# Performance work log

Measured on AMD Instinct MI355X. Metric: run time of the kernel, lower is better.

The kernel has to match this reference:

```python
import jax, jax.numpy as jnp
import numpy as np

D, H, C = 128, 128, 10
N, M, T = 256, 128, 128
DELTA = 1.0
SIGMA2 = 1.0
JITTER = 1e-3


def _net(params, x):
    # x: (D,) -> (C,)   2-hidden-layer tanh MLP (the `network` of NTKSVGP)
    W1, b1, W2, b2, W3, b3 = params
    h = jnp.tanh(x @ W1 + b1)
    h = jnp.tanh(h @ W2 + b2)
    return h @ W3 + b3


def _flat_jac(params, X):
    # per-sample jacobian wrt all params, flattened over params: (B, C, P)
    jac = jax.vmap(lambda x: jax.jacrev(_net)(params, x))(X)
    leaves = jax.tree_util.tree_leaves(jac)
    return jnp.concatenate([j.reshape(j.shape[0], j.shape[1], -1) for j in leaves], axis=-1)


def _forward(X, Y, Z, X_test, W1, b1, W2, b2, W3, b3):
    params = (W1, b1, W2, b2, W3, b3)
    scale = 1.0 / (DELTA * N)  # build_ntk: 1/(delta*num_data)

    Jx = _flat_jac(params, X)       # (N, C, P)
    Jz = _flat_jac(params, Z)       # (M, C, P)
    Jt = _flat_jac(params, X_test)  # (T, C, P)

    Kzx = jnp.einsum('mcp,ncp->cmn', Jz, Jx) * scale   # (C, M, N)
    Kzz = jnp.einsum('mcp,kcp->cmk', Jz, Jz) * scale   # (C, M, M)

    # Gaussian likelihood duals: beta = 2*Hessian = I/sigma2, alpha = -d nll/df = (Y-F)/sigma2
    F = jax.vmap(_net, in_axes=(None, 0))(params, X)   # (N, C)
    beta_diag = jnp.ones_like(F) / SIGMA2              # (N, C)
    alpha = (Y - F) / SIGMA2
    Lam = alpha + F * beta_diag                        # calc_lambda

    # beta_u = Kzx diag(beta) Kzx^T ; Lambda_u = Kzx Lambda
    beta_u = jnp.einsum('cmn,nc,ckn->cmk', Kzx, beta_diag, Kzx)  # (C, M, M)
    Lambda_u = jnp.einsum('cmn,nc->cm', Kzx, Lam)                # (C, M)

    Iz = jnp.eye(M, dtype=Kzz.dtype)
    Kzz_j = Kzz + JITTER * Iz
    KzzB = Kzz_j + beta_u + JITTER * Iz
    alpha_u = jnp.linalg.solve(KzzB, Lambda_u[..., None])[..., 0]  # (C, M)

    # predict_from_sparse_duals (full_cov=False branch)
    Lm = jnp.linalg.cholesky(Kzz_j)  # lower, batched over C
    Lb = jnp.linalg.cholesky(KzzB)
    Kxz = jnp.einsum('tcp,mcp->ctm', Jt, Jz) * scale  # (C, T, M)
    Kxx_diag = jnp.einsum('tcp,tcp->ct', Jt, Jt) * scale  # (C, T)

    f_mean = jnp.einsum('ctm,cm->tc', Kxz, alpha_u)   # (T, C)
    Kzxt = jnp.swapaxes(Kxz, -1, -2)                  # (C, M, T)
    Am = jax.scipy.linalg.solve_triangular(Lm, Kzxt, lower=True)
    Ab = jax.scipy.linalg.solve_triangular(Lb, Kzxt, lower=True)
    f_var = Kxx_diag - jnp.sum(Am * Am, axis=-2) + jnp.sum(Ab * Ab, axis=-2)  # (C, T)
    return jnp.stack([f_mean, f_var.T])  # (2, T, C)


def setup_inputs() -> dict:
    key = jax.random.key(0)
    ks = jax.random.split(key, 8)
    return {
        'X': jax.random.normal(ks[0], (N, D), jnp.float32),
        'Y': jax.random.normal(ks[1], (N, C), jnp.float32),
        'Z': jax.random.normal(ks[2], (M, D), jnp.float32),
        'X_test': jax.random.normal(ks[3], (T, D), jnp.float32),
        'W1': jax.random.normal(ks[4], (D, H), jnp.float32) / np.sqrt(D),
        'b1': jnp.zeros((H,), jnp.float32),
        'W2': jax.random.normal(ks[5], (H, H), jnp.float32) / np.sqrt(H),
        'b2': jnp.zeros((H,), jnp.float32),
        'W3': jax.random.normal(ks[6], (H, C), jnp.float32) / np.sqrt(H),
        'b3': jnp.zeros((C,), jnp.float32),
    }


def reference(X, Y, Z, X_test, W1, b1, W2, b2, W3, b3):
    return _forward(X, Y, Z, X_test, W1, b1, W2, b2, W3, b3)
```

## Files before the change

### kernel.cpp

```cpp
#include <hip/hip_runtime.h>

#define H 128
#define DD 128
#define CC 10
#define NX 256
#define MZ 128
#define TN 128
#define S_TOT 512
#define SCALE (1.0f/256.0f)
#define JIT 1e-3f
#define INV_S2 1.0f

#define OFF_XS    0u
#define OFF_A1    (OFF_XS   + S_TOT*DD)
#define OFF_A2    (OFF_A1   + S_TOT*H)
#define OFF_G1    (OFF_A2   + S_TOT*H)
#define OFF_G2    (OFF_G1   + S_TOT*CC*H)
#define OFF_BASE  (OFF_G2   + S_TOT*CC*H)
#define BASE_ZX   0u
#define BASE_ZZ   (3u*MZ*NX)
#define BASE_TZ   (3u*MZ*NX + 3u*MZ*MZ)
#define OFF_KZX   (OFF_BASE + 3u*MZ*NX + 3u*MZ*MZ + 3u*TN*MZ)
#define OFF_KZZ   (OFF_KZX  + CC*MZ*NX)
#define OFF_KXZ   (OFF_KZZ  + CC*MZ*MZ)
#define OFF_KZZJ  (OFF_KXZ  + CC*TN*MZ)
#define OFF_KZZB  (OFF_KZZJ + CC*MZ*MZ)
#define OFF_LAMU  (OFF_KZZB + CC*MZ*MZ)
#define OFF_LC    (OFF_LAMU + CC*MZ)
#define OFF_INVD  (OFF_LC   + 2u*CC*MZ*MZ)
#define OFF_YLAM  (OFF_INVD + 2u*CC*MZ)

#define WRED(val, qi) { float v_ = (val);                                     \
  v_ += __shfl_down(v_,32,64); v_ += __shfl_down(v_,16,64);                   \
  v_ += __shfl_down(v_, 8,64); v_ += __shfl_down(v_, 4,64);                   \
  v_ += __shfl_down(v_, 2,64); v_ += __shfl_down(v_, 1,64);                   \
  if ((h & 63) == 0) partG[(qi)*2 + (h>>6)] = v_; }

__global__ __launch_bounds__(128) void k_features(
    const float* __restrict__ X, const float* __restrict__ Z, const float* __restrict__ Xt,
    const float* __restrict__ W1, const float* __restrict__ b1,
    const float* __restrict__ W2, const float* __restrict__ b2,
    const float* __restrict__ W3,
    float* __restrict__ XS, float* __restrict__ A1, float* __restrict__ A2,
    float* __restrict__ G1, float* __restrict__ G2, float* __restrict__ LamU,
    float* __restrict__ out)
{
  int s = blockIdx.x, h = threadIdx.x;
  __shared__ float xs[DD], a1s[H], g2s[CC*H];
  __shared__ float w2t[H*129];
  __shared__ float partG[46];
  if (s == 0) {
    #pragma unroll
    for (int c = 0; c < CC; ++c) LamU[c*MZ + h] = 0.0f;
  }
  const float* xin = (s < NX) ? X + s*DD : (s < NX+MZ ? Z + (s-NX)*DD : Xt + (s-NX-MZ)*DD);
  float xv = xin[h];
  xs[h] = xv; XS[s*DD + h] = xv;
  {
    const float4* W2_4 = (const float4*)W2;
    #pragma unroll 4
    for (int it = 0; it < 32; ++it) {
      int f = it*128 + h;
      int r = f >> 5;
      int q = f & 31;
      float4 v = W2_4[f];
      w2t[(4*q+0)*129 + r] = v.x;
      w2t[(4*q+1)*129 + r] = v.y;
      w2t[(4*q+2)*129 + r] = v.z;
      w2t[(4*q+3)*129 + r] = v.w;
    }
  }
  __syncthreads();
  float acc = b1[h];
  #pragma unroll 8
  for (int d0 = 0; d0 < DD; ++d0) acc += xs[d0] * W1[d0*H + h];
  float a1 = tanhf(acc);
  a1s[h] = a1; A1[s*H + h] = a1;
  __syncthreads();
  acc = b2[h];
  #pragma unroll 8
  for (int d0 = 0; d0 < H; ++d0) acc += a1s[d0] * w2t[h*129 + d0];
  float a2 = tanhf(acc);
  A2[s*H + h] = a2;
  float t2 = 1.0f - a2*a2;
  float g2v[CC];
  #pragma unroll
  for (int c = 0; c < CC; ++c) {
    g2v[c] = W3[h*CC + c] * t2;
    g2s[c*H + h] = g2v[c];
    G2[(s*CC + c)*H + h] = g2v[c];
  }
  __syncthreads();
  float t1 = 1.0f - a1*a1;
  float accs[CC];
  #pragma unroll
  for (int c = 0; c < CC; ++c) accs[c] = 0.0f;
  #pragma unroll 4
  for (int k = 0; k < H; ++k) {
    float w = w2t[k*129 + h];
    #pragma unroll
    for (int c = 0; c < CC; ++c) accs[c] += w * g2s[c*H + k];
  }
  #pragma unroll
  for (int c = 0; c < CC; ++c) G1[(s*CC + c)*H + h] = t1 * accs[c];
  if (s >= NX + MZ) {
    int t = s - NX - MZ;
    WRED(xv*xv, 0) WRED(a1*a1, 1) WRED(a2*a2, 2)
    #pragma unroll
    for (int c = 0; c < CC; ++c) {
      float g1v = t1 * accs[c];
      WRED(g1v*g1v, 3+2*c)
      WRED(g2v[c]*g2v[c], 4+2*c)
    }
    __syncthreads();
    if (h < CC) {
      int c = h;
      float nx  = partG[0] + partG[1];
      float na1 = partG[2] + partG[3];
      float na2 = partG[4] + partG[5];
      float n1 = partG[(3+2*c)*2] + partG[(3+2*c)*2+1];
      float n2 = partG[(4+2*c)*2] + partG[(4+2*c)*2+1];
      out[TN*CC + t*CC + c] = SCALE * ((1.0f+nx)*n1 + (1.0f+na1)*n2 + (1.0f+na2));
    }
  }
}

__global__ __launch_bounds__(256) void k_base(const float* __restrict__ XS,
    const float* __restrict__ A1, const float* __restrict__ A2, float* __restrict__ Base)
{
  int set = blockIdx.z;
  int colsN = (set == 0) ? NX : MZ;
  if ((int)blockIdx.x * 16 >= colsN) return;
  int rowOff = (set == 2) ? NX+MZ : NX;
  int colOff = (set == 0) ? 0 : NX;
  unsigned baseOff = (set == 0) ? BASE_ZX : (set == 1 ? BASE_ZZ : BASE_TZ);
  __shared__ float rx[16*132], r1[16*132], r2[16*132], cxs[16*132], c1s[16*132], c2s[16*132];
  int tid = threadIdx.x, m0 = blockIdx.y*16, n0 = blockIdx.x*16;
  for (int idx = tid; idx < 16*128; idx += 256) {
    int r = idx >> 7, hh = idx & 127;
    int sr = rowOff + m0 + r, sc = colOff + n0 + r;
    rx [r*132+hh] = XS[sr*DD+hh]; r1[r*132+hh] = A1[sr*H+hh]; r2[r*132+hh] = A2[sr*H+hh];
    cxs[r*132+hh] = XS[sc*DD+hh]; c1s[r*132+hh] = A1[sc*H+hh]; c2s[r*132+hh] = A2[sc*H+hh];
  }
  __syncthreads();
  int ty = tid >> 4, tx = tid & 15;
  const float4* pa = (const float4*)(rx  + ty*132);
  const float4* pb = (const float4*)(cxs + tx*132);
  const float4* pc = (const float4*)(r1  + ty*132);
  const float4* pd = (const float4*)(c1s + tx*132);
  const float4* pe = (const float4*)(r2  + ty*132);
  const float4* pf = (const float4*)(c2s + tx*132);
  float d0 = 0, d1 = 0, d2 = 0;
  #pragma unroll 8
  for (int q = 0; q < 32; ++q) {
    float4 a = pa[q], b = pb[q]; d0 += a.x*b.x + a.y*b.y + a.z*b.z + a.w*b.w;
    float4 c = pc[q], d = pd[q]; d1 += c.x*d.x + c.y*d.y + c.z*d.z + c.w*d.w;
    float4 e = pe[q], f = pf[q]; d2 += e.x*f.x + e.y*f.y + e.z*f.z + e.w*f.w;
  }
  int m = m0 + ty, n = n0 + tx;
  float* Bp = Base + baseOff;
  int area = 128 * colsN;
  Bp[0*area + m*colsN + n] = 1.0f + d0;
  Bp[1*area + m*colsN + n] = 1.0f + d1;
  Bp[2*area + m*colsN + n] = 1.0f + d2;
}

__global__ __launch_bounds__(256) void k_gram(const float* __restrict__ G1, const float* __restrict__ G2,
    const float* __restrict__ Base, const float* __restrict__ Y,
    float* __restrict__ Kzx, float* __restrict__ Kzz, float* __restrict__ Kxz,
    float* __restrict__ LamU)
{
  int z = blockIdx.z, set = z / CC, c = z % CC;
  int colsN = (set == 0) ? NX : MZ;
  if ((int)blockIdx.x * 16 >= colsN) return;
  int rowOff = (set == 2) ? NX+MZ : NX;
  int colOff = (set == 0) ? 0 : NX;
  unsigned baseOff = (set == 0) ? BASE_ZX : (set == 1 ? BASE_ZZ : BASE_TZ);
  float* outp = (set == 0) ? Kzx + c*MZ*NX : (set == 1 ? Kzz + c*MZ*MZ : Kxz + c*TN*MZ);
  __shared__ float g1r[16*132], g2r[16*132], g1c[16*132], g2c[16*132];
  int tid = threadIdx.x, m0 = blockIdx.y*16, n0 = blockIdx.x*16;
  for (int idx = tid; idx < 2048; idx += 256) {
    int r = idx >> 7, hh = idx & 127;
    int sr = rowOff + m0 + r, sc = colOff + n0 + r;
    g1r[r*132+hh] = G1[(sr*CC + c)*H + hh]; g2r[r*132+hh] = G2[(sr*CC + c)*H + hh];
    g1c[r*132+hh] = G1[(sc*CC + c)*H + hh]; g2c[r*132+hh] = G2[(sc*CC + c)*H + hh];
  }
  __syncthreads();
  int ty = tid >> 4, tx = tid & 15;
  const float4* p1 = (const float4*)(g1r + ty*132);
  const float4* p2 = (const float4*)(g1c + tx*132);
  const float4* p3 = (const float4*)(g2r + ty*132);
  const float4* p4 = (const float4*)(g2c + tx*132);
  float dg1 = 0, dg2 = 0;
  #pragma unroll 8
  for (int q = 0; q < 32; ++q) {
    float4 a = p1[q], b = p2[q]; dg1 += a.x*b.x + a.y*b.y + a.z*b.z + a.w*b.w;
    float4 e = p3[q], f = p4[q]; dg2 += e.x*f.x + e.y*f.y + e.z*f.z + e.w*f.w;
  }
  int m = m0 + ty, n = n0 + tx;
  const float* Bp = Base + baseOff;
  int area = 128 * colsN;
  float b0 = Bp[m*colsN + n], b1v = Bp[area + m*colsN + n], b2v = Bp[2*area + m*colsN + n];
  float val = SCALE * (b0*dg1 + b1v*dg2 + b2v);
  outp[m*colsN + n] = val;
  if (set == 0) {
    float lam = val * Y[n*CC + c] * INV_S2;
    lam += __shfl_xor(lam, 1, 64); lam += __shfl_xor(lam, 2, 64);
    lam += __shfl_xor(lam, 4, 64); lam += __shfl_xor(lam, 8, 64);
    if (tx == 0) atomicAdd(&LamU[c*MZ + m], lam);
  }
}

__global__ __launch_bounds__(256) void k_kzzb(const float* __restrict__ Kzx, const float* __restrict__ Kzz,
    float* __restrict__ Kzzj, float* __restrict__ KzzB)
{
  int c = blockIdx.z, m0 = blockIdx.y*16, k0 = blockIdx.x*16;
  int tid = threadIdx.x, ty = tid >> 4, tx = tid & 15;
  __shared__ float Am[16*260], Ak[16*260];
  const float* Kc = Kzx + c*MZ*NX;
  const float4* src_m = (const float4*)(Kc + m0*NX);
  const float4* src_k = (const float4*)(Kc + k0*NX);
  float4* Am4 = (float4*)Am;
  float4* Ak4 = (float4*)Ak;
  for (int idx = tid; idx < 16*64; idx += 256) {
    int r = idx >> 6, q = idx & 63;
    Am4[r*65 + q] = src_m[r*64 + q];
    Ak4[r*65 + q] = src_k[r*64 + q];
  }
  __syncthreads();
  const float4* am = (const float4*)(Am + ty*260);
  const float4* ak = (const float4*)(Ak + tx*260);
  float acc = 0;
  #pragma unroll 8
  for (int q = 0; q < 64; ++q) {
    float4 a = am[q], b = ak[q];
    acc += a.x*b.x + a.y*b.y + a.z*b.z + a.w*b.w;
  }
  int m = m0+ty, k = k0+tx, idx = c*MZ*MZ + m*MZ + k;
  float kzz = Kzz[idx];
  float dia = (m == k) ? 1.0f : 0.0f;
  Kzzj[idx] = kzz + dia*JIT;
  KzzB[idx] = kzz + acc*INV_S2 + dia*2.0f*JIT;
}

__global__ __launch_bounds__(512) void k_chol(const float* __restrict__ Kzzj, const float* __restrict__ KzzB,
    float* __restrict__ Lc, float* __restrict__ invd,
    const float* __restrict__ LamU, float* __restrict__ ylam)
{
  int which = blockIdx.x & 1, c = blockIdx.x >> 1;
  const float* Ain = (which ? KzzB : Kzzj) + c*MZ*MZ;
  float* LcB = Lc + (size_t)(which*CC + c)*MZ*MZ;
  float* invB = invd + (which*CC + c)*MZ;
  __shared__ float As[MZ*MZ];
  __shared__ float4 pan[MZ];
  __shared__ float bs[MZ];
  __shared__ float ys[MZ];
  int tid = threadIdx.x;
  int rg = tid & 31, kp = tid >> 5;
  float4* As4 = (float4*)As;
  {
    float4* d4 = (float4*)As; const float4* s4 = (const float4*)Ain;
    #pragma unroll
    for (int r = 0; r < 8; ++r) d4[tid + 512*r] = s4[tid + 512*r];
  }
  if (tid < MZ) bs[tid] = which ? LamU[c*MZ + tid] : 0.0f;
  __syncthreads();
  for (int jb = 0; jb < 32; ++jb) {
    int j = jb*4;
    if (tid < MZ) {
      int i = tid;
      float r0 = As[(j+0)*MZ + i], r1 = As[(j+1)*MZ + i], r2 = As[(j+2)*MZ + i], r3 = As[(j+3)*MZ + i];
      float a00 = As[j*MZ+j];
      float a10 = As[j*MZ+j+1], a20 = As[j*MZ+j+2], a30 = As[j*MZ+j+3];
      float a11 = As[(j+1)*MZ+j+1], a21 = As[(j+1)*MZ+j+2], a31 = As[(j+1)*MZ+j+3];
      float a22 = As[(j+2)*MZ+j+2], a32 = As[(j+2)*MZ+j+3];
      float a33 = As[(j+3)*MZ+j+3];
      float bj0 = bs[j], bj1 = bs[j+1], bj2 = bs[j+2], bj3 = bs[j+3];
      float id0 = rsqrtf(a00);
      float l10 = a10*id0, l20 = a20*id0, l30 = a30*id0;
      float id1 = rsqrtf(a11 - l10*l10);
      float l21 = (a21 - l20*l10)*id1, l31 = (a31 - l30*l10)*id1;
      float id2 = rsqrtf(a22 - l20*l20 - l21*l21);
      float l32 = (a32 - l30*l20 - l31*l21)*id2;
      float id3 = rsqrtf(a33 - l30*l30 - l31*l31 - l32*l32);
      float c0 = r0*id0;
      float c1 = (r1 - c0*l10)*id1;
      float c2 = (r2 - c0*l20 - c1*l21)*id2;
      float c3 = (r3 - c0*l30 - c1*l31 - c2*l32)*id3;
      float y0 = bj0*id0;
      float y1 = (bj1 - l10*y0)*id1;
      float y2 = (bj2 - l20*y0 - l21*y1)*id2;
      float y3 = (bj3 - l30*y0 - l31*y1 - l32*y2)*id3;
      pan[i] = make_float4(c0, c1, c2, c3);
      LcB[(j+0)*MZ + i] = (i > j+0) ? c0 : 0.0f;
      LcB[(j+1)*MZ + i] = (i > j+1) ? c1 : 0.0f;
      LcB[(j+2)*MZ + i] = (i > j+2) ? c2 : 0.0f;
      LcB[(j+3)*MZ + i] = (i > j+3) ? c3 : 0.0f;
      if (i == j) {
        invB[j] = id0; invB[j+1] = id1; invB[j+2] = id2; invB[j+3] = id3;
        ys[j] = y0; ys[j+1] = y1; ys[j+2] = y2; ys[j+3] = y3;
      }
      if (i >= j+4) bs[i] -= c0*y0 + c1*y1 + c2*y2 + c3*y3;
    }
    __syncthreads();
    float4 p0 = pan[4*rg+0], p1 = pan[4*rg+1], p2 = pan[4*rg+2], p3 = pan[4*rg+3];
    int kstart = (j + 4) + ((kp - (j + 4)) & 15);
    int kend = 4*rg + 3;
    for (int k = kstart; k <= kend; k += 16) {
      float4 ck = pan[k];
      float4 a4 = As4[k*32 + rg];
      a4.x -= p0.x*ck.x + p0.y*ck.y + p0.z*ck.z + p0.w*ck.w;
      a4.y -= p1.x*ck.x + p1.y*ck.y + p1.z*ck.z + p1.w*ck.w;
      a4.z -= p2.x*ck.x + p2.y*ck.y + p2.z*ck.z + p2.w*ck.w;
      a4.w -= p3.x*ck.x + p3.y*ck.y + p3.z*ck.z + p3.w*ck.w;
      As4[k*32 + rg] = a4;
    }
    __syncthreads();
  }
  if (which && tid < MZ) ylam[c*MZ + tid] = ys[tid];
}

__device__ __forceinline__ float rdlane(float v, int lane) {
  return __int_as_float(__builtin_amdgcn_readlane(__float_as_int(v), lane));
}

__global__ __launch_bounds__(512) void k_solve(const float* __restrict__ Lc,
    const float* __restrict__ invd, const float* __restrict__ ylam,
    const float* __restrict__ Kxz, float* __restrict__ out)
{
  int quarter = blockIdx.x & 3;
  int which   = (blockIdx.x >> 2) & 1;
  int c       = blockIdx.x >> 3;
  const float2* LcB2 = (const float2*)(Lc + (size_t)(which*CC + c)*MZ*MZ);
  const float2* invB2 = (const float2*)(invd + (which*CC + c)*MZ);
  const float2* ylB2  = (const float2*)(ylam + c*MZ);
  int tid = threadIdx.x, l = tid & 63, wv = tid >> 6;
  __shared__ float2 Ls[MZ*64];
  #pragma unroll
  for (int r = 0; r < 16; ++r) Ls[tid + 512*r] = LcB2[tid + 512*r];
  float2 iv = invB2[l];
  float2 yl = ylB2[l];
  int col0 = quarter*32 + wv*4;
  const float* K0 = Kxz + (size_t)c*TN*MZ;
  float2 b0 = *(const float2*)(K0 + (size_t)(col0+0)*MZ + 2*l);
  float2 b1 = *(const float2*)(K0 + (size_t)(col0+1)*MZ + 2*l);
  float2 b2 = *(const float2*)(K0 + (size_t)(col0+2)*MZ + 2*l);
  float2 b3 = *(const float2*)(K0 + (size_t)(col0+3)*MZ + 2*l);
  __syncthreads();
  #pragma unroll
  for (int j = 0; j < MZ; ++j) {
    const int owner = j >> 1;
    float2 Lj = Ls[j*64 + l];
    float y0, y1, y2, y3;
    if ((j & 1) == 0) {
      y0 = rdlane(b0.x * iv.x, owner);
      y1 = rdlane(b1.x * iv.x, owner);
      y2 = rdlane(b2.x * iv.x, owner);
      y3 = rdlane(b3.x * iv.x, owner);
    } else {
      y0 = rdlane(b0.y * iv.y, owner);
      y1 = rdlane(b1.y * iv.y, owner);
      y2 = rdlane(b2.y * iv.y, owner);
      y3 = rdlane(b3.y * iv.y, owner);
    }
    b0.x -= Lj.x * y0; b0.y -= Lj.y * y0;
    b1.x -= Lj.x * y1; b1.y -= Lj.y * y1;
    b2.x -= Lj.x * y2; b2.y -= Lj.y * y2;
    b3.x -= Lj.x * y3; b3.y -= Lj.y * y3;
    if (l == owner) {
      if ((j & 1) == 0) { b0.x = y0; b1.x = y1; b2.x = y2; b3.x = y3; }
      else              { b0.y = y0; b1.y = y1; b2.y = y2; b3.y = y3; }
    }
  }
  float sq0 = b0.x*b0.x + b0.y*b0.y, fm0 = b0.x*yl.x + b0.y*yl.y;
  float sq1 = b1.x*b1.x + b1.y*b1.y, fm1 = b1.x*yl.x + b1.y*yl.y;
  float sq2 = b2.x*b2.x + b2.y*b2.y, fm2 = b2.x*yl.x + b2.y*yl.y;
  float sq3 = b3.x*b3.x + b3.y*b3.y, fm3 = b3.x*yl.x + b3.y*yl.y;
  #pragma unroll
  for (int off = 32; off > 0; off >>= 1) {
    sq0 += __shfl_xor(sq0, off, 64); fm0 += __shfl_xor(fm0, off, 64);
    sq1 += __shfl_xor(sq1, off, 64); fm1 += __shfl_xor(fm1, off, 64);
    sq2 += __shfl_xor(sq2, off, 64); fm2 += __shfl_xor(fm2, off, 64);
    sq3 += __shfl_xor(sq3, off, 64); fm3 += __shfl_xor(fm3, off, 64);
  }
  if (l == 0) {
    float sgn = which ? 1.0f : -1.0f;
    float* var = out + TN*CC;
    atomicAdd(&var[(col0+0)*CC + c], sgn*sq0);
    atomicAdd(&var[(col0+1)*CC + c], sgn*sq1);
    atomicAdd(&var[(col0+2)*CC + c], sgn*sq2);
    atomicAdd(&var[(col0+3)*CC + c], sgn*sq3);
    if (which) {
      out[(col0+0)*CC + c] = fm0;
      out[(col0+1)*CC + c] = fm1;
      out[(col0+2)*CC + c] = fm2;
      out[(col0+3)*CC + c] = fm3;
    }
  }
}

extern "C" void kernel_launch(void* const* d_in, const int* in_sizes, int n_in,
                              void* d_out, int out_size, void* d_ws, size_t ws_size,
                              hipStream_t stream) {
  (void)in_sizes; (void)n_in; (void)out_size; (void)ws_size;
  const float* X  = (const float*)d_in[0];
  const float* Y  = (const float*)d_in[1];
  const float* Z  = (const float*)d_in[2];
  const float* Xt = (const float*)d_in[3];
  const float* W1 = (const float*)d_in[4];
  const float* b1 = (const float*)d_in[5];
  const float* W2 = (const float*)d_in[6];
  const float* b2 = (const float*)d_in[7];
  const float* W3 = (const float*)d_in[8];
  float* ws  = (float*)d_ws;
  float* out = (float*)d_out;

  float* XS   = ws + OFF_XS;
  float* A1   = ws + OFF_A1;
  float* A2   = ws + OFF_A2;
  float* G1   = ws + OFF_G1;
  float* G2   = ws + OFF_G2;
  float* Base = ws + OFF_BASE;
  float* Kzx  = ws + OFF_KZX;
  float* Kzz  = ws + OFF_KZZ;
  float* Kxz  = ws + OFF_KXZ;
  float* Kzzj = ws + OFF_KZZJ;
  float* KzzB = ws + OFF_KZZB;
  float* LamU = ws + OFF_LAMU;
  float* Lc   = ws + OFF_LC;
  float* invd = ws + OFF_INVD;
  float* ylam = ws + OFF_YLAM;

  k_features<<<S_TOT, 128, 0, stream>>>(X, Z, Xt, W1, b1, W2, b2, W3, XS, A1, A2, G1, G2, LamU, out);
  k_base<<<dim3(16, 8, 3), 256, 0, stream>>>(XS, A1, A2, Base);
  k_gram<<<dim3(16, 8, 3*CC), 256, 0, stream>>>(G1, G2, Base, Y, Kzx, Kzz, Kxz, LamU);
  k_kzzb<<<dim3(8, 8, CC), 256, 0, stream>>>(Kzx, Kzz, Kzzj, KzzB);
  k_chol<<<2*CC, 512, 0, stream>>>(Kzzj, KzzB, Lc, invd, LamU, ylam);
  k_solve<<<8*CC, 512, 0, stream>>>(Lc, invd, ylam, Kxz, out);
}
```

Baseline: 120.9 us.

## Process two samples per block in features kernel and 2x2 register tile gram kernel

k_features now handles two samples per 256-thread block, so each block loads and transposes W2 into shared memory once for two samples instead of once per sample. k_gram switches from 16x16 to 32x32 output tiles, with each thread computing a 2x2 block of outputs, so every shared-memory float4 load is reused twice and the number of blocks re-staging G1/G2 rows drops. The cost is more registers and shared memory per block and fewer blocks overall, which may reduce occupancy and parallelism on a GPU with many CUs.

```diff
diff --git a/kernel.cpp b/kernel.cpp
--- a/kernel.cpp
+++ b/kernel.cpp
@@ -36,7 +36,7 @@
   v_ += __shfl_down(v_, 2,64); v_ += __shfl_down(v_, 1,64);                   \
   if ((h & 63) == 0) partG[(qi)*2 + (h>>6)] = v_; }
 
-__global__ __launch_bounds__(128) void k_features(
+__global__ __launch_bounds__(256) void k_features(
     const float* __restrict__ X, const float* __restrict__ Z, const float* __restrict__ Xt,
     const float* __restrict__ W1, const float* __restrict__ b1,
     const float* __restrict__ W2, const float* __restrict__ b2,
@@ -45,22 +45,25 @@
     float* __restrict__ G1, float* __restrict__ G2, float* __restrict__ LamU,
     float* __restrict__ out)
 {
-  int s = blockIdx.x, h = threadIdx.x;
-  __shared__ float xs[DD], a1s[H], g2s[CC*H];
+  int b = blockIdx.x, tid = threadIdx.x;
+  int g = tid >> 7, h = tid & 127;
+  int s = 2*b + g;
   __shared__ float w2t[H*129];
-  __shared__ float partG[46];
-  if (s == 0) {
+  __shared__ float xs[2][DD], a1s[2][H], g2s[2][CC*H];
+  __shared__ float partGA[2][46];
+  float* partG = partGA[g];
+  if (b == 0 && tid < 128) {
     #pragma unroll
-    for (int c = 0; c < CC; ++c) LamU[c*MZ + h] = 0.0f;
+    for (int c = 0; c < CC; ++c) LamU[c*MZ + tid] = 0.0f;
   }
   const float* xin = (s < NX) ? X + s*DD : (s < NX+MZ ? Z + (s-NX)*DD : Xt + (s-NX-MZ)*DD);
   float xv = xin[h];
-  xs[h] = xv; XS[s*DD + h] = xv;
+  xs[g][h] = xv; XS[s*DD + h] = xv;
   {
     const float4* W2_4 = (const float4*)W2;
     #pragma unroll 4
-    for (int it = 0; it < 32; ++it) {
-      int f = it*128 + h;
+    for (int it = 0; it < 16; ++it) {
+      int f = it*256 + tid;
       int r = f >> 5;
       int q = f & 31;
       float4 v = W2_4[f];
@@ -73,13 +76,13 @@
   __syncthreads();
   float acc = b1[h];
   #pragma unroll 8
-  for (int d0 = 0; d0 < DD; ++d0) acc += xs[d0] * W1[d0*H + h];
+  for (int d0 = 0; d0 < DD; ++d0) acc += xs[g][d0] * W1[d0*H + h];
   float a1 = tanhf(acc);
-  a1s[h] = a1; A1[s*H + h] = a1;
+  a1s[g][h] = a1; A1[s*H + h] = a1;
   __syncthreads();
   acc = b2[h];
   #pragma unroll 8
-  for (int d0 = 0; d0 < H; ++d0) acc += a1s[d0] * w2t[h*129 + d0];
+  for (int d0 = 0; d0 < H; ++d0) acc += a1s[g][d0] * w2t[h*129 + d0];
   float a2 = tanhf(acc);
   A2[s*H + h] = a2;
   float t2 = 1.0f - a2*a2;
@@ -87,7 +90,7 @@
   #pragma unroll
   for (int c = 0; c < CC; ++c) {
     g2v[c] = W3[h*CC + c] * t2;
-    g2s[c*H + h] = g2v[c];
+    g2s[g][c*H + h] = g2v[c];
     G2[(s*CC + c)*H + h] = g2v[c];
   }
   __syncthreads();
@@ -99,12 +102,11 @@
   for (int k = 0; k < H; ++k) {
     float w = w2t[k*129 + h];
     #pragma unroll
-    for (int c = 0; c < CC; ++c) accs[c] += w * g2s[c*H + k];
+    for (int c = 0; c < CC; ++c) accs[c] += w * g2s[g][c*H + k];
   }
   #pragma unroll
   for (int c = 0; c < CC; ++c) G1[(s*CC + c)*H + h] = t1 * accs[c];
-  if (s >= NX + MZ) {
-    int t = s - NX - MZ;
+  if (b >= 192) {
     WRED(xv*xv, 0) WRED(a1*a1, 1) WRED(a2*a2, 2)
     #pragma unroll
     for (int c = 0; c < CC; ++c) {
@@ -113,13 +115,15 @@
       WRED(g2v[c]*g2v[c], 4+2*c)
     }
     __syncthreads();
-    if (h < CC) {
-      int c = h;
-      float nx  = partG[0] + partG[1];
-      float na1 = partG[2] + partG[3];
-      float na2 = partG[4] + partG[5];
-      float n1 = partG[(3+2*c)*2] + partG[(3+2*c)*2+1];
-      float n2 = partG[(4+2*c)*2] + partG[(4+2*c)*2+1];
+    if (tid < 2*CC) {
+      int gi = tid / CC, c = tid % CC;
+      const float* P = partGA[gi];
+      float nx  = P[0] + P[1];
+      float na1 = P[2] + P[3];
+      float na2 = P[4] + P[5];
+      float n1 = P[(3+2*c)*2] + P[(3+2*c)*2+1];
+      float n2 = P[(4+2*c)*2] + P[(4+2*c)*2+1];
+      int t = 2*(b-192) + gi;
       out[TN*CC + t*CC + c] = SCALE * ((1.0f+nx)*n1 + (1.0f+na1)*n2 + (1.0f+na2));
     }
   }
@@ -172,14 +176,14 @@
 {
   int z = blockIdx.z, set = z / CC, c = z % CC;
   int colsN = (set == 0) ? NX : MZ;
-  if ((int)blockIdx.x * 16 >= colsN) return;
+  if ((int)blockIdx.x * 32 >= colsN) return;
   int rowOff = (set == 2) ? NX+MZ : NX;
   int colOff = (set == 0) ? 0 : NX;
   unsigned baseOff = (set == 0) ? BASE_ZX : (set == 1 ? BASE_ZZ : BASE_TZ);
   float* outp = (set == 0) ? Kzx + c*MZ*NX : (set == 1 ? Kzz + c*MZ*MZ : Kxz + c*TN*MZ);
-  __shared__ float g1r[16*132], g2r[16*132], g1c[16*132], g2c[16*132];
-  int tid = threadIdx.x, m0 = blockIdx.y*16, n0 = blockIdx.x*16;
-  for (int idx = tid; idx < 2048; idx += 256) {
+  __shared__ float g1r[32*132], g2r[32*132], g1c[32*132], g2c[32*132];
+  int tid = threadIdx.x, m0 = blockIdx.y*32, n0 = blockIdx.x*32;
+  for (int idx = tid; idx < 32*128; idx += 256) {
     int r = idx >> 7, hh = idx & 127;
     int sr = rowOff + m0 + r, sc = colOff + n0 + r;
     g1r[r*132+hh] = G1[(sr*CC + c)*H + hh]; g2r[r*132+hh] = G2[(sr*CC + c)*H + hh];
@@ -187,27 +191,58 @@
   }
   __syncthreads();
   int ty = tid >> 4, tx = tid & 15;
-  const float4* p1 = (const float4*)(g1r + ty*132);
-  const float4* p2 = (const float4*)(g1c + tx*132);
-  const float4* p3 = (const float4*)(g2r + ty*132);
-  const float4* p4 = (const float4*)(g2c + tx*132);
-  float dg1 = 0, dg2 = 0;
-  #pragma unroll 8
+  const float4* a0p = (const float4*)(g1r + ty*132);
+  const float4* a1p = (const float4*)(g1r + (ty+16)*132);
+  const float4* b0p = (const float4*)(g1c + tx*132);
+  const float4* b1p = (const float4*)(g1c + (tx+16)*132);
+  const float4* e0p = (const float4*)(g2r + ty*132);
+  const float4* e1p = (const float4*)(g2r + (ty+16)*132);
+  const float4* f0p = (const float4*)(g2c + tx*132);
+  const float4* f1p = (const float4*)(g2c + (tx+16)*132);
+  float d1_00=0, d1_01=0, d1_10=0, d1_11=0;
+  float d2_00=0, d2_01=0, d2_10=0, d2_11=0;
+  #pragma unroll 4
   for (int q = 0; q < 32; ++q) {
-    float4 a = p1[q], b = p2[q]; dg1 += a.x*b.x + a.y*b.y + a.z*b.z + a.w*b.w;
-    float4 e = p3[q], f = p4[q]; dg2 += e.x*f.x + e.y*f.y + e.z*f.z + e.w*f.w;
-  }
-  int m = m0 + ty, n = n0 + tx;
+    float4 a0 = a0p[q], a1 = a1p[q], b0 = b0p[q], b1 = b1p[q];
+    d1_00 += a0.x*b0.x + a0.y*b0.y + a0.z*b0.z + a0.w*b0.w;
+    d1_01 += a0.x*b1.x + a0.y*b1.y + a0.z*b1.z + a0.w*b1.w;
+    d1_10 += a1.x*b0.x + a1.y*b0.y + a1.z*b0.z + a1.w*b0.w;
+    d1_11 += a1.x*b1.x + a1.y*b1.y + a1.z*b1.z + a1.w*b1.w;
+    float4 e0 = e0p[q], e1 = e1p[q], f0 = f0p[q], f1 = f1p[q];
+    d2_00 += e0.x*f0.x + e0.y*f0.y + e0.z*f0.z + e0.w*f0.w;
+    d2_01 += e0.x*f1.x + e0.y*f1.y + e0.z*f1.z + e0.w*f1.w;
+    d2_10 += e1.x*f0.x + e1.y*f0.y + e1.z*f0.z + e1.w*f0.w;
+    d2_11 += e1.x*f1.x + e1.y*f1.y + e1.z*f1.z + e1.w*f1.w;
+  }
   const float* Bp = Base + baseOff;
   int area = 128 * colsN;
-  float b0 = Bp[m*colsN + n], b1v = Bp[area + m*colsN + n], b2v = Bp[2*area + m*colsN + n];
-  float val = SCALE * (b0*dg1 + b1v*dg2 + b2v);
-  outp[m*colsN + n] = val;
+  int mA = m0 + ty, mB = m0 + ty + 16, nA = n0 + tx, nB = n0 + tx + 16;
+  float v00, v01, v10, v11;
+  {
+    float b0v = Bp[mA*colsN + nA], b1v = Bp[area + mA*colsN + nA], b2v = Bp[2*area + mA*colsN + nA];
+    v00 = SCALE * (b0v*d1_00 + b1v*d2_00 + b2v);
+    b0v = Bp[mA*colsN + nB]; b1v = Bp[area + mA*colsN + nB]; b2v = Bp[2*area + mA*colsN + nB];
+    v01 = SCALE * (b0v*d1_01 + b1v*d2_01 + b2v);
+    b0v = Bp[mB*colsN + nA]; b1v = Bp[area + mB*colsN + nA]; b2v = Bp[2*area + mB*colsN + nA];
+    v10 = SCALE * (b0v*d1_10 + b1v*d2_10 + b2v);
+    b0v = Bp[mB*colsN + nB]; b1v = Bp[area + mB*colsN + nB]; b2v = Bp[2*area + mB*colsN + nB];
+    v11 = SCALE * (b0v*d1_11 + b1v*d2_11 + b2v);
+  }
+  outp[mA*colsN + nA] = v00;
+  outp[mA*colsN + nB] = v01;
+  outp[mB*colsN + nA] = v10;
+  outp[mB*colsN + nB] = v11;
   if (set == 0) {
-    float lam = val * Y[n*CC + c] * INV_S2;
-    lam += __shfl_xor(lam, 1, 64); lam += __shfl_xor(lam, 2, 64);
-    lam += __shfl_xor(lam, 4, 64); lam += __shfl_xor(lam, 8, 64);
-    if (tx == 0) atomicAdd(&LamU[c*MZ + m], lam);
+    float lamA = v00 * Y[nA*CC + c] + v01 * Y[nB*CC + c];
+    float lamB = v10 * Y[nA*CC + c] + v11 * Y[nB*CC + c];
+    lamA += __shfl_xor(lamA, 1, 64); lamA += __shfl_xor(lamA, 2, 64);
+    lamA += __shfl_xor(lamA, 4, 64); lamA += __shfl_xor(lamA, 8, 64);
+    lamB += __shfl_xor(lamB, 1, 64); lamB += __shfl_xor(lamB, 2, 64);
+    lamB += __shfl_xor(lamB, 4, 64); lamB += __shfl_xor(lamB, 8, 64);
+    if (tx == 0) {
+      atomicAdd(&LamU[c*MZ + mA], lamA * INV_S2);
+      atomicAdd(&LamU[c*MZ + mB], lamB * INV_S2);
+    }
   }
 }
 
@@ -431,9 +466,9 @@
   float* invd = ws + OFF_INVD;
   float* ylam = ws + OFF_YLAM;
 
-  k_features<<<S_TOT, 128, 0, stream>>>(X, Z, Xt, W1, b1, W2, b2, W3, XS, A1, A2, G1, G2, LamU, out);
+  k_features<<<S_TOT/2, 256, 0, stream>>>(X, Z, Xt, W1, b1, W2, b2, W3, XS, A1, A2, G1, G2, LamU, out);
   k_base<<<dim3(16, 8, 3), 256, 0, stream>>>(XS, A1, A2, Base);
-  k_gram<<<dim3(16, 8, 3*CC), 256, 0, stream>>>(G1, G2, Base, Y, Kzx, Kzz, Kxz, LamU);
+  k_gram<<<dim3(8, 4, 3*CC), 256, 0, stream>>>(G1, G2, Base, Y, Kzx, Kzz, Kxz, LamU);
   k_kzzb<<<dim3(8, 8, CC), 256, 0, stream>>>(Kzx, Kzz, Kzzj, KzzB);
   k_chol<<<2*CC, 512, 0, stream>>>(Kzzj, KzzB, Lc, invd, LamU, ylam);
   k_solve<<<8*CC, 512, 0, stream>>>(Lc, invd, ylam, Kxz, out);
```

Measured after the change: 116.9 us. 3.3% less time.
